# Kernel optimization log

Measured on AMD Instinct MI355X. Metric: run time of the kernel, lower is better.

## Reference

```python
import jax, jax.numpy as jnp
import numpy as np
from jax import lax

EPS = 1e-5


def fps(xyz, npoint):
    # Farthest point sampling; xyz [B, N, 3] -> idx [B, npoint] (starts at point 0)
    B, N, _ = xyz.shape

    def body(carry, _):
        dist, far = carry
        c = jnp.take_along_axis(xyz, far[:, None, None], axis=1)  # [B,1,3]
        d = jnp.sum((xyz - c) ** 2, -1)                            # [B,N]
        dist = jnp.minimum(dist, d)
        nxt = jnp.argmax(dist, -1).astype(jnp.int32)
        return (dist, nxt), far

    init = (jnp.full((B, N), 1e10, xyz.dtype), jnp.zeros((B,), jnp.int32))
    _, idx = lax.scan(body, init, None, length=npoint)
    return idx.T  # [B, npoint]


def query_ball(radius, nsample, xyz, new_xyz):
    # xyz [B,N,3], new_xyz [B,S,3] -> idx [B,S,nsample]
    N = xyz.shape[1]
    sqr = jnp.sum((new_xyz[:, :, None, :] - xyz[:, None, :, :]) ** 2, -1)  # [B,S,N]
    idx = jnp.where(sqr > radius * radius, N, jnp.arange(N)[None, None, :])
    idx = jnp.sort(idx, axis=-1)[:, :, :nsample]
    # out-of-ball slots get replaced by the first in-ball index (torch repo behavior)
    return jnp.where(idx == N, idx[:, :, :1], idx)


def gather_pts(x, idx):
    # x [B,N,C], idx [B,...] -> [B,...,C]
    B = x.shape[0]
    b = jnp.arange(B).reshape((B,) + (1,) * (idx.ndim - 1))
    return x[b, idx]


def mlp_bn(x, layers):
    # x [B,S,K,C]; shared 1x1-conv MLP + training-mode BatchNorm + ReLU
    for w, g, b in layers:
        x = jnp.einsum('bskc,oc->bsko', x, w)
        mean = x.mean((0, 1, 2))
        var = x.var((0, 1, 2))  # biased, as torch BN uses for normalization
        x = jax.nn.relu((x - mean) * lax.rsqrt(var + EPS) * g + b)
    return x


def set_abstraction(xyz, points, npoint, radius, nsample, layers, group_all):
    B = xyz.shape[0]
    if group_all:
        new_xyz = jnp.zeros((B, 1, 3), xyz.dtype)
        new_points = xyz[:, None]  # [B,1,N,3] (raw xyz, no centering)
        if points is not None:
            new_points = jnp.concatenate([new_points, points[:, None]], -1)
    else:
        fidx = fps(xyz, npoint)
        new_xyz = gather_pts(xyz, fidx)                     # [B,S,3]
        idx = query_ball(radius, nsample, xyz, new_xyz)     # [B,S,K]
        grouped = gather_pts(xyz, idx) - new_xyz[:, :, None, :]
        if points is not None:
            new_points = jnp.concatenate([grouped, gather_pts(points, idx)], -1)
        else:
            new_points = grouped
    feat = mlp_bn(new_points, layers).max(2)  # max-pool over neighbors -> [B,S,C]
    return new_xyz, feat


def _forward(xyz_time, l1, l2, l3):
    B, T, N, _ = xyz_time.shape
    x = xyz_time.reshape(B * T, N, 4)
    xyz, t = x[..., :3], x[..., 3:]
    x1_xyz, x1 = set_abstraction(xyz, t, 512, 0.2, 32, l1, False)
    x2_xyz, x2 = set_abstraction(x1_xyz, x1, 128, 0.4, 64, l2, False)
    _, x3 = set_abstraction(x2_xyz, x2, None, None, None, l3, True)
    return x3.reshape(B, T, -1)


def setup_inputs() -> dict:
    key = jax.random.key(0)
    ks = jax.random.split(key, 16)
    inp = {"xyz_time": jax.random.uniform(ks[0], (2, 4, 4096, 4), jnp.float32)}
    specs = {1: [(64, 4), (64, 64), (128, 64)],
             2: [(128, 131), (128, 128), (256, 128)],
             3: [(256, 259), (512, 256), (1024, 512)]}
    i = 1
    for s, layers in specs.items():
        for j, (o, c) in enumerate(layers):
            inp[f"w{s}_{j}"] = jax.random.normal(jax.random.fold_in(ks[i], j), (o, c), jnp.float32) * 0.1
            inp[f"g{s}_{j}"] = jnp.ones((o,), jnp.float32)
            inp[f"b{s}_{j}"] = jnp.zeros((o,), jnp.float32)
        i += 1
    return inp


def reference(xyz_time, w1_0, g1_0, b1_0, w1_1, g1_1, b1_1, w1_2, g1_2, b1_2,
              w2_0, g2_0, b2_0, w2_1, g2_1, b2_1, w2_2, g2_2, b2_2,
              w3_0, g3_0, b3_0, w3_1, g3_1, b3_1, w3_2, g3_2, b3_2):
    l1 = [(w1_0, g1_0, b1_0), (w1_1, g1_1, b1_1), (w1_2, g1_2, b1_2)]
    l2 = [(w2_0, g2_0, b2_0), (w2_1, g2_1, b2_1), (w2_2, g2_2, b2_2)]
    l3 = [(w3_0, g3_0, b3_0), (w3_1, g3_1, b3_1), (w3_2, g3_2, b3_2)]
    return _forward(xyz_time, l1, l2, l3)
```

## Files before the change

### kernel.cpp

```cpp
#include <hip/hip_runtime.h>


typedef short s16x8 __attribute__((ext_vector_type(8)));
typedef float f32x4 __attribute__((ext_vector_type(4)));

__device__ __forceinline__ unsigned short f2bf_rne(float f) {
    unsigned u = __float_as_uint(f);
    u += 0x7FFFu + ((u >> 16) & 1u);
    return (unsigned short)(u >> 16);
}
__device__ __forceinline__ void f2bf_split(float v, unsigned short& hi,
                                           unsigned short& lo) {
    unsigned u = __float_as_uint(v);
    unsigned r = u + 0x7FFFu + ((u >> 16) & 1u);
    hi = (unsigned short)(r >> 16);
    float vh = __uint_as_float(r & 0xFFFF0000u);
    lo = f2bf_rne(v - vh);
}

__device__ __forceinline__ unsigned long long umax64(unsigned long long a,
                                                     unsigned long long b) {
    return a > b ? a : b;
}

__device__ __forceinline__ unsigned wred_umax63(unsigned v) {
    unsigned t;
    t = (unsigned)__builtin_amdgcn_update_dpp(0, (int)v, 0x111, 0xf, 0xf, true); if (t > v) v = t;
    t = (unsigned)__builtin_amdgcn_update_dpp(0, (int)v, 0x112, 0xf, 0xf, true); if (t > v) v = t;
    t = (unsigned)__builtin_amdgcn_update_dpp(0, (int)v, 0x114, 0xf, 0xf, true); if (t > v) v = t;
    t = (unsigned)__builtin_amdgcn_update_dpp(0, (int)v, 0x118, 0xf, 0xf, true); if (t > v) v = t;
    t = (unsigned)__builtin_amdgcn_update_dpp(0, (int)v, 0x142, 0xa, 0xf, true); if (t > v) v = t;
    t = (unsigned)__builtin_amdgcn_update_dpp(0, (int)v, 0x143, 0xc, 0xf, true); if (t > v) v = t;
    return v;
}

__device__ __forceinline__ void wave_argmax(unsigned dbits, unsigned nInv,
                                            unsigned& vmax, unsigned& iInv) {
    unsigned m = wred_umax63(dbits);
    vmax = (unsigned)__builtin_amdgcn_readlane((int)m, 63);
    unsigned cand = (dbits == vmax) ? nInv : 0u;
    unsigned im = wred_umax63(cand);
    iInv = (unsigned)__builtin_amdgcn_readlane((int)im, 63);
}

struct PWArgs {
    const float* w[9];
    unsigned off[9];
    int O[9], C[9], CP[9];
};
__device__ __forceinline__ void prep_w_dev(const PWArgs& a,
                                           unsigned short* __restrict__ wh,
                                           unsigned short* __restrict__ wl,
                                           int i) {
    int l = 0;
#pragma unroll
    for (int k = 1; k < 9; ++k) if (i >= (int)a.off[k]) l = k;
    int li = i - (int)a.off[l];
    int CP = a.CP[l];
    int o = li / CP;
    int c = li - o * CP;
    float v = (c < a.C[l]) ? a.w[l][(size_t)o * a.C[l] + c] : 0.f;
    unsigned short h, lo;
    f2bf_split(v, h, lo);
    wh[i] = h; wl[i] = lo;
}

template<int NT, int ITEMS, int STRIDE>
__global__ __launch_bounds__(NT) void fps_block(
    const float* __restrict__ pts, int npoint,
    int* __restrict__ outIdx, float* __restrict__ outXyz,
    int nFps, PWArgs pw, unsigned short* __restrict__ wh,
    unsigned short* __restrict__ wl, int wtotal)
{
    constexpr int N = NT * ITEMS;
    constexpr int NW = NT / 64;
    __shared__ float4 scoord[N];
    __shared__ unsigned long long wkey[2][NW];

    if (blockIdx.x >= nFps) {
        int i = (blockIdx.x - nFps) * NT + threadIdx.x;
        if (i < wtotal) prep_w_dev(pw, wh, wl, i);
        return;
    }

    const int b = blockIdx.x;
    const int tid = threadIdx.x;
    const int wid = tid >> 6;
    const int lane = tid & 63;
    const float* P = pts + (size_t)b * N * STRIDE;

    float px[ITEMS], py[ITEMS], pz[ITEMS], dloc[ITEMS];
#pragma unroll
    for (int w = 0; w < ITEMS; ++w) {
        int n = tid + w * NT;
        float x, y, z;
        if (STRIDE == 4) {
            float4 v = *(const float4*)(P + (size_t)n * 4);
            x = v.x; y = v.y; z = v.z;
        } else {
            x = P[(size_t)n * STRIDE + 0];
            y = P[(size_t)n * STRIDE + 1];
            z = P[(size_t)n * STRIDE + 2];
        }
        px[w] = x; py[w] = y; pz[w] = z;
        scoord[n] = make_float4(x, y, z, 0.f);
        dloc[w] = 1e10f;
    }
    __syncthreads();
    float4 c0 = scoord[0];
    float cx = c0.x, cy = c0.y, cz = c0.z;
    int far = 0;

    for (int i = 0; i < npoint; ++i) {
        if (tid == 0) {
            outIdx[(size_t)b * npoint + i] = far;
            outXyz[((size_t)b * npoint + i) * 3 + 0] = cx;
            outXyz[((size_t)b * npoint + i) * 3 + 1] = cy;
            outXyz[((size_t)b * npoint + i) * 3 + 2] = cz;
        }
        float bestV = -1.0f;
        int bestW = 0;
#pragma unroll
        for (int w = 0; w < ITEMS; ++w) {
            float dx = __fsub_rn(px[w], cx);
            float dy = __fsub_rn(py[w], cy);
            float dz = __fsub_rn(pz[w], cz);
            float d = __fadd_rn(__fadd_rn(__fmul_rn(dx, dx), __fmul_rn(dy, dy)),
                                __fmul_rn(dz, dz));
            float dd = fminf(dloc[w], d);
            dloc[w] = dd;
            if (dd > bestV) { bestV = dd; bestW = w; }
        }
        int bestN = tid + bestW * NT;
        unsigned vmax, iInv;
        wave_argmax(__float_as_uint(bestV), 0xFFFFFFFFu ^ (unsigned)bestN,
                    vmax, iInv);
        const int par = i & 1;
        if (lane == 0)
            wkey[par][wid] = ((unsigned long long)vmax << 32) | iInv;
        __syncthreads();
        unsigned long long kb = wkey[par][0];
#pragma unroll
        for (int w2 = 1; w2 < NW; ++w2) kb = umax64(kb, wkey[par][w2]);
        far = (int)(0xFFFFFFFFu ^ (unsigned)kb);
        float4 cc = scoord[far];
        cx = cc.x; cy = cc.y; cz = cc.z;
    }
}

__device__ void fps_wave_dev(const float* __restrict__ pts, int npoint,
                             int* __restrict__ outIdx, float* __restrict__ outXyz,
                             int b, float4* scoord)
{
    constexpr int ITEMS = 8;
    constexpr int STRIDE = 3;
    constexpr int N = 64 * ITEMS;
    const int tid = threadIdx.x;
    const float* P = pts + (size_t)b * N * STRIDE;

    float px[ITEMS], py[ITEMS], pz[ITEMS], dloc[ITEMS];
#pragma unroll
    for (int w = 0; w < ITEMS; ++w) {
        int n = tid + w * 64;
        float x = P[(size_t)n * STRIDE + 0];
        float y = P[(size_t)n * STRIDE + 1];
        float z = P[(size_t)n * STRIDE + 2];
        px[w] = x; py[w] = y; pz[w] = z;
        scoord[n] = make_float4(x, y, z, 0.f);
        dloc[w] = 1e10f;
    }
    __threadfence_block();
    float4 c0 = scoord[0];
    float cx = c0.x, cy = c0.y, cz = c0.z;
    int far = 0;

    for (int i = 0; i < npoint; ++i) {
        if (tid == 0) {
            outIdx[(size_t)b * npoint + i] = far;
            outXyz[((size_t)b * npoint + i) * 3 + 0] = cx;
            outXyz[((size_t)b * npoint + i) * 3 + 1] = cy;
            outXyz[((size_t)b * npoint + i) * 3 + 2] = cz;
        }
        float bestV = -1.0f;
        int bestW = 0;
#pragma unroll
        for (int w = 0; w < ITEMS; ++w) {
            float dx = __fsub_rn(px[w], cx);
            float dy = __fsub_rn(py[w], cy);
            float dz = __fsub_rn(pz[w], cz);
            float d = __fadd_rn(__fadd_rn(__fmul_rn(dx, dx), __fmul_rn(dy, dy)),
                                __fmul_rn(dz, dz));
            float dd = fminf(dloc[w], d);
            dloc[w] = dd;
            if (dd > bestV) { bestV = dd; bestW = w; }
        }
        int bestN = tid + bestW * 64;
        unsigned vmax, iInv;
        wave_argmax(__float_as_uint(bestV), 0xFFFFFFFFu ^ (unsigned)bestN,
                    vmax, iInv);
        far = (int)(0xFFFFFFFFu ^ iInv);
        float4 cc = scoord[far];
        cx = cc.x; cy = cc.y; cz = cc.z;
    }
}

__global__ __launch_bounds__(256) void qb_group1(
    const float* __restrict__ xyz ,
    const float* __restrict__ ctr ,
    const float* __restrict__ W0 ,
    float* __restrict__ Yout ,
    double* __restrict__ pS0, double* __restrict__ pQ0,
    int nQb, const float* __restrict__ fpsPts,
    int* __restrict__ fpsIdx, float* __restrict__ fpsXyz)
{
    __shared__ float4 scoord[512];
    __shared__ float4 srows[4][32];
    __shared__ float sstat[4][64][2];
    if ((int)blockIdx.x >= nQb) {
        if (threadIdx.x < 64)
            fps_wave_dev(fpsPts, 128, fpsIdx, fpsXyz,
                         (int)blockIdx.x - nQb, scoord);
        return;
    }
    const int tid = threadIdx.x;
    const int gw = (blockIdx.x * 256 + tid) >> 6;
    const int wid = tid >> 6;
    const int lane = tid & 63;
    int b = gw >> 9;
    const float* P = xyz + (size_t)b * 4096 * 4;
    float cx = ctr[(size_t)gw * 3 + 0];
    float cy = ctr[(size_t)gw * 3 + 1];
    float cz = ctr[(size_t)gw * 3 + 2];
    int cnt = 0;
    float f0x = 0.f, f0y = 0.f, f0z = 0.f, f0t = 0.f;
    bool haveFirst = false;
    for (int base = 0; base < 4096 && cnt < 32; base += 64) {
        int n = base + lane;
        float4 p = *(const float4*)(P + (size_t)n * 4);
        float ex = __fsub_rn(p.x, cx);
        float ey = __fsub_rn(p.y, cy);
        float ez = __fsub_rn(p.z, cz);
        float d = __fadd_rn(__fadd_rn(__fmul_rn(ex, ex), __fmul_rn(ey, ey)),
                            __fmul_rn(ez, ez));
        bool inb = !(d > 0.04f);
        unsigned long long mask = __ballot(inb);
        if (mask) {
            if (!haveFirst) {
                int fl = (int)__builtin_ctzll(mask);
                f0x = __shfl(ex, fl); f0y = __shfl(ey, fl);
                f0z = __shfl(ez, fl); f0t = __shfl(p.w, fl);
                haveFirst = true;
            }
            if (inb) {
                int pos = cnt + __builtin_popcountll(mask & ((1ull << lane) - 1ull));
                if (pos < 32)
                    srows[wid][pos] = make_float4(ex, ey, ez, p.w);
            }
            cnt += (int)__builtin_popcountll(mask);
        }
    }
    if (cnt > 32) cnt = 32;
    for (int p2 = cnt + lane; p2 < 32; p2 += 64)
        srows[wid][p2] = make_float4(f0x, f0y, f0z, f0t);
    __syncthreads();

    float wc0 = W0[lane * 4 + 0];
    float wc1 = W0[lane * 4 + 1];
    float wc2 = W0[lane * 4 + 2];
    float wc3 = W0[lane * 4 + 3];
    float s = 0.f, s2 = 0.f;
    float* yp = Yout + (size_t)gw * 32 * 64 + lane;
#pragma unroll 4
    for (int r = 0; r < 32; ++r) {
        float4 e = srows[wid][r];
        float y = e.x * wc0 + e.y * wc1 + e.z * wc2 + e.w * wc3;
        yp[(size_t)r * 64] = y;
        s += y;
        s2 += y * y;
    }
    sstat[wid][lane][0] = s;
    sstat[wid][lane][1] = s2;
    __syncthreads();
    if (tid < 64) {
        double S = 0.0, S2 = 0.0;
#pragma unroll
        for (int w2 = 0; w2 < 4; ++w2) {
            S += (double)sstat[w2][tid][0];
            S2 += (double)sstat[w2][tid][1];
        }
        atomicAdd(&pS0[tid], S);
        atomicAdd(&pQ0[tid], S2);
    }
}

__device__ __forceinline__ void qb2_dev(
    const float* __restrict__ xyz, const float* __restrict__ centers,
    int* __restrict__ outIdx, int gw, int lane)
{
    const int N = 512, stride = 3, S = 128, nsample = 64;
    const float r2 = 0.16f;
    int b = gw / S;
    const float* P = xyz + (size_t)b * N * stride;
    float cx = centers[(size_t)gw * 3 + 0];
    float cy = centers[(size_t)gw * 3 + 1];
    float cz = centers[(size_t)gw * 3 + 2];
    int* out = outIdx + (size_t)gw * nsample;
    int cnt = 0;
    int firstIdx = 0;
    bool haveFirst = false;
    for (int base = 0; base < N && cnt < nsample; base += 64) {
        int n = base + lane;
        bool inb = false;
        if (n < N) {
            float dx = __fsub_rn(cx, P[(size_t)n * stride + 0]);
            float dy = __fsub_rn(cy, P[(size_t)n * stride + 1]);
            float dz = __fsub_rn(cz, P[(size_t)n * stride + 2]);
            float d = __fadd_rn(__fadd_rn(__fmul_rn(dx, dx), __fmul_rn(dy, dy)),
                                __fmul_rn(dz, dz));
            inb = !(d > r2);
        }
        unsigned long long mask = __ballot(inb);
        if (mask) {
            if (!haveFirst) { firstIdx = base + __builtin_ctzll(mask); haveFirst = true; }
            if (inb) {
                int pos = cnt + __builtin_popcountll(mask & ((1ull << lane) - 1ull));
                if (pos < nsample) out[pos] = n;
            }
            cnt += (int)__builtin_popcountll(mask);
        }
    }
    if (cnt > nsample) cnt = nsample;
    for (int p = cnt + lane; p < nsample; p += 64) out[p] = firstIdx;
}

__global__ __launch_bounds__(256) void gemm_fused(
    const float* __restrict__ X,
    const double* __restrict__ pSin, const double* __restrict__ pQin,
    const float* __restrict__ gIn, const float* __restrict__ bIn,
    double invMin, int actMode, int bnCh,
    const unsigned short* __restrict__ Bh, const unsigned short* __restrict__ Bl,
    float* __restrict__ Y,
    double* __restrict__ pSout, double* __restrict__ pQout,
    int AC, int CPW, int O, int gmode,
    const int* __restrict__ gqb, const float* __restrict__ gxyz,
    const float* __restrict__ gctr, const float* __restrict__ gfeat,
    const float* __restrict__ gfmin,
    int redK, float* __restrict__ Vmax, float* __restrict__ Vmin,
    int nMain, const float* __restrict__ qbXyz,
    const float* __restrict__ qbCtr, int* __restrict__ qbOut)
{
    constexpr int PITCH = 40;
    __shared__ __align__(16) unsigned short sAh[128 * PITCH];
    __shared__ __align__(16) unsigned short sAl[128 * PITCH];
    __shared__ __align__(16) unsigned short sBh[128 * PITCH];
    __shared__ __align__(16) unsigned short sBl[128 * PITCH];
    __shared__ float sred[2048];
    __shared__ float sScale[512];
    __shared__ float sShift[512];

    if ((int)blockIdx.x >= nMain) {
        int wid = threadIdx.x >> 6, lane = threadIdx.x & 63;
        int gw = ((int)blockIdx.x - nMain) * 4 + wid;
        if (gw < 1024) qb2_dev(qbXyz, qbCtr, qbOut, gw, lane);
        return;
    }

    const int tid = threadIdx.x;
    const int lane = tid & 63;
    const int wid = tid >> 6;
    const int col15 = lane & 15;
    const int quad = lane >> 4;
    const int wm = (wid >> 1) * 64;
    const int wo = (wid & 1) * 64;
    const int m0 = blockIdx.x * 128;
    const int o0 = blockIdx.y * 128;
    const int lr = tid >> 2;
    const int lc = (tid & 3) * 8;

    if (bnCh > 0) {
        for (int c = tid; c < bnCh; c += 256) {
            double S = pSin[c], Q = pQin[c];
            double mean = S * invMin;
            double var = Q * invMin - mean * mean;
            float varf = (float)var;
            if (varf < 0.f) varf = 0.f;
            float sc = gIn[c] * rsqrtf(varf + 1e-5f);
            sScale[c] = sc;
            sShift[c] = bIn[c] - (float)mean * sc;
        }
    }
    __syncthreads();

    f32x4 acc[4][4];
#pragma unroll
    for (int mt = 0; mt < 4; ++mt)
#pragma unroll
        for (int ot = 0; ot < 4; ++ot)
            acc[mt][ot] = {0.f, 0.f, 0.f, 0.f};

    for (int k0 = 0; k0 < CPW; k0 += 32) {
#pragma unroll
        for (int it = 0; it < 2; ++it) {
            int r = lr + it * 64;
            int c = k0 + lc;
            unsigned short h[8], l[8];
            float vv[8];
            bool have = true;
            if (gmode == 0) {
                if (c + 8 <= AC) {
                    const float* xr = X + (size_t)(m0 + r) * AC + c;
                    float4 v0 = *(const float4*)xr;
                    float4 v1 = *(const float4*)(xr + 4);
                    vv[0] = v0.x; vv[1] = v0.y; vv[2] = v0.z; vv[3] = v0.w;
                    vv[4] = v1.x; vv[5] = v1.y; vv[6] = v1.z; vv[7] = v1.w;
                    if (actMode == 1) {
#pragma unroll
                        for (int j = 0; j < 8; ++j)
                            vv[j] = fmaxf(vv[j] * sScale[c + j] + sShift[c + j], 0.f);
                    }
                } else {
                    have = false;
                }
            } else if (gmode == 2) {
                int m = m0 + r;
                int idx = gqb[m];
                idx = (idx < 0) ? 0 : (idx > 511 ? 511 : idx);
                int bb2 = m >> 13;
                int bs = m >> 6;
                int ctrg = bb2 * 512 + idx;
                const float* fmx = gfeat + (size_t)ctrg * 128;
                const float* fmn = gfmin + (size_t)ctrg * 128;
                const float* xrow = gxyz + (size_t)ctrg * 3;
                const float* crow = gctr + (size_t)bs * 3;
#pragma unroll
                for (int j = 0; j < 8; ++j) {
                    int cc = c + j;
                    float v = 0.f;
                    if (cc < 3)        v = __fsub_rn(xrow[cc], crow[cc]);
                    else if (cc < 131) {
                        int fc = cc - 3;
                        float sc = sScale[fc];
                        float sel = (sc >= 0.f) ? fmx[fc] : fmn[fc];
                        v = fmaxf(sel * sc + sShift[fc], 0.f);
                    }
                    vv[j] = v;
                }
            } else {
                int m = m0 + r;
                const float* fmx = gfeat + (size_t)m * 256;
                const float* fmn = gfmin + (size_t)m * 256;
                const float* crow = gctr + (size_t)m * 3;
#pragma unroll
                for (int j = 0; j < 8; ++j) {
                    int cc = c + j;
                    float v = 0.f;
                    if (cc < 3)        v = crow[cc];
                    else if (cc < 259) {
                        int fc = cc - 3;
                        float sc = sScale[fc];
                        float sel = (sc >= 0.f) ? fmx[fc] : fmn[fc];
                        v = fmaxf(sel * sc + sShift[fc], 0.f);
                    }
                    vv[j] = v;
                }
            }
            if (have) {
#pragma unroll
                for (int j = 0; j < 8; ++j) f2bf_split(vv[j], h[j], l[j]);
            } else {
#pragma unroll
                for (int j = 0; j < 8; ++j) { h[j] = 0; l[j] = 0; }
            }
            *(ushort4*)&sAh[r * PITCH + lc] = make_ushort4(h[0], h[1], h[2], h[3]);
            *(ushort4*)&sAh[r * PITCH + lc + 4] = make_ushort4(h[4], h[5], h[6], h[7]);
            *(ushort4*)&sAl[r * PITCH + lc] = make_ushort4(l[0], l[1], l[2], l[3]);
            *(ushort4*)&sAl[r * PITCH + lc + 4] = make_ushort4(l[4], l[5], l[6], l[7]);
        }
#pragma unroll
        for (int it = 0; it < 2; ++it) {
            int r = lr + it * 64;
            int c = k0 + lc;
            int o = o0 + r;
            uint4 vh = {0, 0, 0, 0}, vl = {0, 0, 0, 0};
            if (o < O && c < CPW) {
                size_t goff = (size_t)o * CPW + c;
                vh = *(const uint4*)(Bh + goff);
                vl = *(const uint4*)(Bl + goff);
            }
            *(uint4*)&sBh[r * PITCH + lc] = vh;
            *(uint4*)&sBl[r * PITCH + lc] = vl;
        }
        __syncthreads();
        s16x8 ah[4], al[4], bh[4], bl[4];
#pragma unroll
        for (int mt = 0; mt < 4; ++mt) {
            int rowoff = (wm + mt * 16 + col15) * PITCH + quad * 8;
            ah[mt] = *(const s16x8*)&sAh[rowoff];
            al[mt] = *(const s16x8*)&sAl[rowoff];
        }
#pragma unroll
        for (int ot = 0; ot < 4; ++ot) {
            int rowoff = (wo + ot * 16 + col15) * PITCH + quad * 8;
            bh[ot] = *(const s16x8*)&sBh[rowoff];
            bl[ot] = *(const s16x8*)&sBl[rowoff];
        }
#pragma unroll
        for (int mt = 0; mt < 4; ++mt)
#pragma unroll
            for (int ot = 0; ot < 4; ++ot) {
                acc[mt][ot] = __builtin_amdgcn_mfma_f32_16x16x32_bf16(
                    ah[mt], bl[ot], acc[mt][ot], 0, 0, 0);
                acc[mt][ot] = __builtin_amdgcn_mfma_f32_16x16x32_bf16(
                    al[mt], bh[ot], acc[mt][ot], 0, 0, 0);
                acc[mt][ot] = __builtin_amdgcn_mfma_f32_16x16x32_bf16(
                    ah[mt], bh[ot], acc[mt][ot], 0, 0, 0);
            }
        __syncthreads();
    }
    if (redK == 0) {
#pragma unroll
        for (int mt = 0; mt < 4; ++mt)
#pragma unroll
            for (int ot = 0; ot < 4; ++ot) {
                int og = o0 + wo + ot * 16 + col15;
                if (og < O) {
#pragma unroll
                    for (int r = 0; r < 4; ++r) {
                        int mg = m0 + wm + mt * 16 + quad * 4 + r;
                        Y[(size_t)mg * O + og] = acc[mt][ot][r];
                    }
                }
            }
    } else if (redK == 32) {
#pragma unroll
        for (int ot = 0; ot < 4; ++ot) {
            int og = o0 + wo + ot * 16 + col15;
#pragma unroll
            for (int cp = 0; cp < 2; ++cp) {
                float mx = acc[2 * cp][ot][0];
                float mn = mx;
#pragma unroll
                for (int mi = 0; mi < 2; ++mi)
#pragma unroll
                    for (int r = 0; r < 4; ++r) {
                        float v = acc[2 * cp + mi][ot][r];
                        mx = fmaxf(mx, v);
                        mn = fminf(mn, v);
                    }
                mx = fmaxf(mx, __shfl_xor(mx, 16));
                mx = fmaxf(mx, __shfl_xor(mx, 32));
                mn = fminf(mn, __shfl_xor(mn, 16));
                mn = fminf(mn, __shfl_xor(mn, 32));
                if (quad == 0) {
                    int ctr = (m0 >> 5) + (wm >> 5) + cp;
                    Vmax[(size_t)ctr * O + og] = mx;
                    Vmin[(size_t)ctr * O + og] = mn;
                }
            }
        }
    } else {
#pragma unroll
        for (int ot = 0; ot < 4; ++ot) {
            int og = o0 + wo + ot * 16 + col15;
            float mx = acc[0][ot][0];
            float mn = mx;
#pragma unroll
            for (int mt = 0; mt < 4; ++mt)
#pragma unroll
                for (int r = 0; r < 4; ++r) {
                    float v = acc[mt][ot][r];
                    mx = fmaxf(mx, v);
                    mn = fminf(mn, v);
                }
            mx = fmaxf(mx, __shfl_xor(mx, 16));
            mx = fmaxf(mx, __shfl_xor(mx, 32));
            mn = fminf(mn, __shfl_xor(mn, 16));
            mn = fminf(mn, __shfl_xor(mn, 32));
            if (quad == 0) {
                int ctr = (m0 >> 6) + (wm >> 6);
                Vmax[(size_t)ctr * O + og] = mx;
                Vmin[(size_t)ctr * O + og] = mn;
            }
        }
    }
#pragma unroll
    for (int ot = 0; ot < 4; ++ot) {
        float s = 0.f, s2 = 0.f;
#pragma unroll
        for (int mt = 0; mt < 4; ++mt)
#pragma unroll
            for (int r = 0; r < 4; ++r) {
                float v = acc[mt][ot][r];
                s += v;
                s2 += v * v;
            }
        int slot = ((wid * 4 + quad) * 16 + col15) * 4 + ot;
        sred[slot * 2] = s;
        sred[slot * 2 + 1] = s2;
    }
    __syncthreads();
    if (tid < 128) {
        int col = tid;
        int o = o0 + col;
        if (o < O) {
            int cb = col >> 6;
            int ot = (col & 63) >> 4;
            int c15 = col & 15;
            double S = 0.0, S2 = 0.0;
#pragma unroll
            for (int wp = 0; wp < 2; ++wp) {
                int wd = cb + wp * 2;
#pragma unroll
                for (int q = 0; q < 4; ++q) {
                    int slot = ((wd * 4 + q) * 16 + c15) * 4 + ot;
                    S += (double)sred[slot * 2];
                    S2 += (double)sred[slot * 2 + 1];
                }
            }
            atomicAdd(&pSout[o], S);
            atomicAdd(&pQout[o], S2);
        }
    }
}

__global__ __launch_bounds__(256) void bn_relu_max(
    const float* __restrict__ Y,
    const double* __restrict__ pS, const double* __restrict__ pQ,
    const float* __restrict__ gv, const float* __restrict__ bv, double invM,
    float* __restrict__ out, int Stot, int K, int O)
{
    int idx = blockIdx.x * 256 + threadIdx.x;
    if (idx >= Stot * O) return;
    int s = idx / O;
    int o = idx - s * O;
    double S = pS[o], Q = pQ[o];
    double mean = S * invM;
    double var = Q * invM - mean * mean;
    float varf = (float)var;
    if (varf < 0.f) varf = 0.f;
    float sc = gv[o] * rsqrtf(varf + 1e-5f);
    float sh = bv[o] - (float)mean * sc;
    const float* basep = Y + (size_t)s * K * O + o;
    float mx = 0.f;
    for (int k = 0; k < K; ++k) {
        float v = basep[(size_t)k * O] * sc + sh;
        v = fmaxf(v, 0.f);
        mx = fmaxf(mx, v);
    }
    out[idx] = mx;
}

extern "C" void kernel_launch(void* const* d_in, const int* in_sizes, int n_in,
                              void* d_out, int out_size, void* d_ws, size_t ws_size,
                              hipStream_t stream)
{
    const float* xin = (const float*)d_in[0];
    const float* w[9]; const float* g[9]; const float* bb[9];
    for (int i = 0; i < 9; ++i) {
        w[i]  = (const float*)d_in[1 + 3 * i];
        g[i]  = (const float*)d_in[2 + 3 * i];
        bb[i] = (const float*)d_in[3 + 3 * i];
    }

    char* base = (char*)d_ws;
    size_t off = 0;
    auto alloc = [&](size_t bytes) -> void* {
        void* p = base + off;
        off = (off + bytes + 255) & ~(size_t)255;
        return p;
    };
    const int OC[9][3] = {{64,4,8},{64,64,64},{128,64,64},
                          {128,131,136},{128,128,128},{256,128,128},
                          {256,259,264},{512,256,256},{1024,512,512}};
    size_t woff[10]; woff[0] = 0;
    for (int i = 0; i < 9; ++i) woff[i + 1] = woff[i] + (size_t)OC[i][0] * OC[i][2];

    int*    fps1   = (int*)alloc((size_t)4096 * 4);
    int*    fps2   = (int*)alloc((size_t)1024 * 4);
    int*    qb2    = (int*)alloc((size_t)65536 * 4);
    float*  nx1    = (float*)alloc((size_t)12288 * 4);
    float*  nx2    = (float*)alloc((size_t)3072 * 4);
    double* partS  = (double*)alloc((size_t)9 * 1024 * 8);
    double* partQ  = (double*)alloc((size_t)9 * 1024 * 8);
    unsigned short* WH = (unsigned short*)alloc(woff[9] * 2);
    unsigned short* WL = (unsigned short*)alloc(woff[9] * 2);
    const size_t zeroBytes = off;
    float*  XG = (float*)alloc((size_t)65536 * 136 * 4);
    float*  A  = (float*)alloc((size_t)16777216 * 4);
    if (off > ws_size) return;

    hipMemsetAsync(d_ws, 0, zeroBytes, stream);

    PWArgs pwa;
    for (int i = 0; i < 9; ++i) {
        pwa.w[i] = w[i]; pwa.off[i] = (unsigned)woff[i];
        pwa.O[i] = OC[i][0]; pwa.C[i] = OC[i][1]; pwa.CP[i] = OC[i][2];
    }
    const int nPrep = (int)((woff[9] + 255) / 256);

    auto gemm = [&](const float* X, int prevLi, double invMprev, int actMode,
                    int bnCh, int li, float* Y, int YB, int OB, int AC,
                    int CPW, int O, int gmode, const int* gqb,
                    const float* gxyz, const float* gctr, const float* gfeat,
                    const float* gfmin, int redK, float* Vmax, float* Vmin,
                    int extraQB, const float* qx, const float* qc, int* qo) {
        gemm_fused<<<dim3(YB + extraQB, OB), 256, 0, stream>>>(
            X,
            prevLi >= 0 ? partS + (size_t)prevLi * 1024 : nullptr,
            prevLi >= 0 ? partQ + (size_t)prevLi * 1024 : nullptr,
            prevLi >= 0 ? g[prevLi] : nullptr,
            prevLi >= 0 ? bb[prevLi] : nullptr,
            invMprev, actMode, bnCh,
            WH + woff[li], WL + woff[li], Y,
            partS + (size_t)li * 1024, partQ + (size_t)li * 1024,
            AC, CPW, O, gmode, gqb, gxyz, gctr, gfeat, gfmin,
            redK, Vmax, Vmin, YB, qx, qc, qo);
    };

    const double inv1 = 1.0 / 131072.0;
    const double inv2 = 1.0 / 65536.0;
    const double inv3 = 1.0 / 1024.0;

    fps_block<256, 16, 4><<<8 + nPrep, 256, 0, stream>>>(
        xin, 512, fps1, nx1, 8, pwa, WH, WL, (int)woff[9]);
    qb_group1<<<1024 + 8, 256, 0, stream>>>(
        xin, nx1, w[0], A, partS + 0, partQ + 0, 1024, nx1, fps2, nx2);

    gemm(A, 0, inv1, 1, 64, 1, XG, 1024, 1, 64, 64, 64, 0,
         nullptr, nullptr, nullptr, nullptr, nullptr, 0, nullptr, nullptr,
         256, nx1, nx2, qb2);
    gemm(XG, 1, inv1, 1, 64, 2, A, 1024, 1, 64, 64, 128, 0,
         nullptr, nullptr, nullptr, nullptr, nullptr, 32, A, A + 524288,
         0, nullptr, nullptr, nullptr);

    gemm(nullptr, 2, inv1, 2, 128, 3, XG, 512, 1, 136, 136, 128, 2,
         qb2, nx1, nx2, A, A + 524288, 0, nullptr, nullptr,
         0, nullptr, nullptr, nullptr);
    gemm(XG, 3, inv2, 1, 128, 4, A, 512, 1, 128, 128, 128, 0,
         nullptr, nullptr, nullptr, nullptr, nullptr, 0, nullptr, nullptr,
         0, nullptr, nullptr, nullptr);
    gemm(A, 4, inv2, 1, 128, 5, XG, 512, 2, 128, 128, 256, 0,
         nullptr, nullptr, nullptr, nullptr, nullptr, 64, XG, XG + 262144,
         0, nullptr, nullptr, nullptr);

    gemm(nullptr, 5, inv2, 2, 256, 6, A, 8, 2, 264, 264, 256, 3,
         nullptr, nullptr, nx2, XG, XG + 262144, 0, nullptr, nullptr,
         0, nullptr, nullptr, nullptr);
    gemm(A, 6, inv3, 1, 256, 7, XG, 8, 4, 256, 256, 512, 0,
         nullptr, nullptr, nullptr, nullptr, nullptr, 0, nullptr, nullptr,
         0, nullptr, nullptr, nullptr);
    gemm(XG, 7, inv3, 1, 512, 8, A, 8, 8, 512, 512, 1024, 0,
         nullptr, nullptr, nullptr, nullptr, nullptr, 0, nullptr, nullptr,
         0, nullptr, nullptr, nullptr);
    bn_relu_max<<<(8 * 1024) / 256, 256, 0, stream>>>(
        A, partS + 8 * 1024, partQ + 8 * 1024, g[8], bb[8], inv3,
        (float*)d_out, 8, 128, 1024);
}
```

Baseline: 774.7 us.

## Fuse SA3 GEMM chain and final max into one cooperative kernel

Replaces the three SA3 MLP GEMM launches and the BN-ReLU-max launch with a single cooperative kernel of 64 blocks. Grid-wide syncs separate the stages, and each block loops over output tiles. This removes per-launch overhead and idle gaps between the small SA3 kernels. The cost is fewer blocks per stage, grid.sync overhead, and a fallback to the old launches if the cooperative launch fails.

```diff
diff --git a/kernel.cpp b/kernel.cpp
--- a/kernel.cpp
+++ b/kernel.cpp
@@ -1,4 +1,7 @@
 #include <hip/hip_runtime.h>
+#include <hip/hip_cooperative_groups.h>
+
+namespace cg = cooperative_groups;
 
 
 typedef short s16x8 __attribute__((ext_vector_type(8)));
@@ -623,6 +626,259 @@
     }
 }
 
+__device__ void sa3_gemm(
+    const float* __restrict__ X,
+    const double* __restrict__ pSin, const double* __restrict__ pQin,
+    const float* __restrict__ gIn, const float* __restrict__ bIn,
+    double invMin, int bnCh, int gmode,
+    const float* __restrict__ gctr, const float* __restrict__ gfeat,
+    const float* __restrict__ gfmin,
+    const unsigned short* __restrict__ Bh, const unsigned short* __restrict__ Bl,
+    float* __restrict__ Y, double* __restrict__ pSout, double* __restrict__ pQout,
+    int AC, int CPW, int O, int YB, int ntile, int G,
+    unsigned short* sAh, unsigned short* sAl,
+    unsigned short* sBh, unsigned short* sBl,
+    float* sred, float* sScale, float* sShift)
+{
+    constexpr int PITCH = 40;
+    const int tid = threadIdx.x;
+    const int lane = tid & 63;
+    const int wid = tid >> 6;
+    const int col15 = lane & 15;
+    const int quad = lane >> 4;
+    const int wm = (wid >> 1) * 64;
+    const int wo = (wid & 1) * 64;
+    const int lr = tid >> 2;
+    const int lc = (tid & 3) * 8;
+
+    for (int c = tid; c < bnCh; c += 256) {
+        double S = pSin[c], Q = pQin[c];
+        double mean = S * invMin;
+        double var = Q * invMin - mean * mean;
+        float varf = (float)var;
+        if (varf < 0.f) varf = 0.f;
+        float sc = gIn[c] * rsqrtf(varf + 1e-5f);
+        sScale[c] = sc;
+        sShift[c] = bIn[c] - (float)mean * sc;
+    }
+    __syncthreads();
+
+    for (int t = blockIdx.x; t < ntile; t += G) {
+        const int m0 = (t % YB) * 128;
+        const int o0 = (t / YB) * 128;
+        f32x4 acc[4][4];
+#pragma unroll
+        for (int mt = 0; mt < 4; ++mt)
+#pragma unroll
+            for (int ot = 0; ot < 4; ++ot) acc[mt][ot] = {0.f, 0.f, 0.f, 0.f};
+
+        for (int k0 = 0; k0 < CPW; k0 += 32) {
+#pragma unroll
+            for (int it = 0; it < 2; ++it) {
+                int r = lr + it * 64;
+                int c = k0 + lc;
+                unsigned short h[8], l[8];
+                float vv[8];
+                bool have = true;
+                if (gmode == 0) {
+                    if (c + 8 <= AC) {
+                        const float* xr = X + (size_t)(m0 + r) * AC + c;
+                        float4 v0 = *(const float4*)xr;
+                        float4 v1 = *(const float4*)(xr + 4);
+                        vv[0] = v0.x; vv[1] = v0.y; vv[2] = v0.z; vv[3] = v0.w;
+                        vv[4] = v1.x; vv[5] = v1.y; vv[6] = v1.z; vv[7] = v1.w;
+#pragma unroll
+                        for (int j = 0; j < 8; ++j)
+                            vv[j] = fmaxf(vv[j] * sScale[c + j] + sShift[c + j], 0.f);
+                    } else {
+                        have = false;
+                    }
+                } else {
+                    int m = m0 + r;
+                    const float* fmx = gfeat + (size_t)m * 256;
+                    const float* fmn = gfmin + (size_t)m * 256;
+                    const float* crow = gctr + (size_t)m * 3;
+#pragma unroll
+                    for (int j = 0; j < 8; ++j) {
+                        int cc = c + j;
+                        float v = 0.f;
+                        if (cc < 3)        v = crow[cc];
+                        else if (cc < 259) {
+                            int fc = cc - 3;
+                            float sc = sScale[fc];
+                            float sel = (sc >= 0.f) ? fmx[fc] : fmn[fc];
+                            v = fmaxf(sel * sc + sShift[fc], 0.f);
+                        }
+                        vv[j] = v;
+                    }
+                }
+                if (have) {
+#pragma unroll
+                    for (int j = 0; j < 8; ++j) f2bf_split(vv[j], h[j], l[j]);
+                } else {
+#pragma unroll
+                    for (int j = 0; j < 8; ++j) { h[j] = 0; l[j] = 0; }
+                }
+                *(ushort4*)&sAh[r * PITCH + lc] = make_ushort4(h[0], h[1], h[2], h[3]);
+                *(ushort4*)&sAh[r * PITCH + lc + 4] = make_ushort4(h[4], h[5], h[6], h[7]);
+                *(ushort4*)&sAl[r * PITCH + lc] = make_ushort4(l[0], l[1], l[2], l[3]);
+                *(ushort4*)&sAl[r * PITCH + lc + 4] = make_ushort4(l[4], l[5], l[6], l[7]);
+            }
+#pragma unroll
+            for (int it = 0; it < 2; ++it) {
+                int r = lr + it * 64;
+                int c = k0 + lc;
+                int o = o0 + r;
+                uint4 vh = {0, 0, 0, 0}, vl = {0, 0, 0, 0};
+                if (o < O && c < CPW) {
+                    size_t goff = (size_t)o * CPW + c;
+                    vh = *(const uint4*)(Bh + goff);
+                    vl = *(const uint4*)(Bl + goff);
+                }
+                *(uint4*)&sBh[r * PITCH + lc] = vh;
+                *(uint4*)&sBl[r * PITCH + lc] = vl;
+            }
+            __syncthreads();
+            s16x8 ah[4], al[4], bh[4], bl[4];
+#pragma unroll
+            for (int mt = 0; mt < 4; ++mt) {
+                int rowoff = (wm + mt * 16 + col15) * PITCH + quad * 8;
+                ah[mt] = *(const s16x8*)&sAh[rowoff];
+                al[mt] = *(const s16x8*)&sAl[rowoff];
+            }
+#pragma unroll
+            for (int ot = 0; ot < 4; ++ot) {
+                int rowoff = (wo + ot * 16 + col15) * PITCH + quad * 8;
+                bh[ot] = *(const s16x8*)&sBh[rowoff];
+                bl[ot] = *(const s16x8*)&sBl[rowoff];
+            }
+#pragma unroll
+            for (int mt = 0; mt < 4; ++mt)
+#pragma unroll
+                for (int ot = 0; ot < 4; ++ot) {
+                    acc[mt][ot] = __builtin_amdgcn_mfma_f32_16x16x32_bf16(
+                        ah[mt], bl[ot], acc[mt][ot], 0, 0, 0);
+                    acc[mt][ot] = __builtin_amdgcn_mfma_f32_16x16x32_bf16(
+                        al[mt], bh[ot], acc[mt][ot], 0, 0, 0);
+                    acc[mt][ot] = __builtin_amdgcn_mfma_f32_16x16x32_bf16(
+                        ah[mt], bh[ot], acc[mt][ot], 0, 0, 0);
+                }
+            __syncthreads();
+        }
+#pragma unroll
+        for (int mt = 0; mt < 4; ++mt)
+#pragma unroll
+            for (int ot = 0; ot < 4; ++ot) {
+                int og = o0 + wo + ot * 16 + col15;
+                if (og < O) {
+#pragma unroll
+                    for (int r = 0; r < 4; ++r) {
+                        int mg = m0 + wm + mt * 16 + quad * 4 + r;
+                        Y[(size_t)mg * O + og] = acc[mt][ot][r];
+                    }
+                }
+            }
+#pragma unroll
+        for (int ot = 0; ot < 4; ++ot) {
+            float s = 0.f, s2 = 0.f;
+#pragma unroll
+            for (int mt = 0; mt < 4; ++mt)
+#pragma unroll
+                for (int r = 0; r < 4; ++r) {
+                    float v = acc[mt][ot][r];
+                    s += v;
+                    s2 += v * v;
+                }
+            int slot = ((wid * 4 + quad) * 16 + col15) * 4 + ot;
+            sred[slot * 2] = s;
+            sred[slot * 2 + 1] = s2;
+        }
+        __syncthreads();
+        if (tid < 128) {
+            int col = tid;
+            int o = o0 + col;
+            if (o < O) {
+                int cb = col >> 6;
+                int ot = (col & 63) >> 4;
+                int c15 = col & 15;
+                double S = 0.0, S2 = 0.0;
+#pragma unroll
+                for (int wp = 0; wp < 2; ++wp) {
+                    int wd = cb + wp * 2;
+#pragma unroll
+                    for (int q = 0; q < 4; ++q) {
+                        int slot = ((wd * 4 + q) * 16 + c15) * 4 + ot;
+                        S += (double)sred[slot * 2];
+                        S2 += (double)sred[slot * 2 + 1];
+                    }
+                }
+                atomicAdd(&pSout[o], S);
+                atomicAdd(&pQout[o], S2);
+            }
+        }
+        __syncthreads();
+    }
+}
+
+struct SA3Args {
+    const float* nx2; const float* Vmax2; const float* Vmin2;
+    const unsigned short *Bh6, *Bl6, *Bh7, *Bl7, *Bh8, *Bl8;
+    double *pS5, *pQ5, *pS6, *pQ6, *pS7, *pQ7, *pS8, *pQ8;
+    const float *g5, *b5, *g6, *b6, *g7, *b7, *g8, *b8;
+    float *bufA, *bufB, *bufC, *out;
+    double inv2, inv3;
+};
+
+__global__ __launch_bounds__(256) void sa3_coop(SA3Args a)
+{
+    constexpr int PITCH = 40;
+    __shared__ __align__(16) unsigned short sAh[128 * PITCH];
+    __shared__ __align__(16) unsigned short sAl[128 * PITCH];
+    __shared__ __align__(16) unsigned short sBh[128 * PITCH];
+    __shared__ __align__(16) unsigned short sBl[128 * PITCH];
+    __shared__ float sred[2048];
+    __shared__ float sScale[512];
+    __shared__ float sShift[512];
+    cg::grid_group grid = cg::this_grid();
+    const int G = gridDim.x;
+
+    sa3_gemm(nullptr, a.pS5, a.pQ5, a.g5, a.b5, a.inv2, 256, 3,
+             a.nx2, a.Vmax2, a.Vmin2, a.Bh6, a.Bl6,
+             a.bufA, a.pS6, a.pQ6, 264, 264, 256, 8, 16, G,
+             sAh, sAl, sBh, sBl, sred, sScale, sShift);
+    grid.sync();
+    sa3_gemm(a.bufA, a.pS6, a.pQ6, a.g6, a.b6, a.inv3, 256, 0,
+             nullptr, nullptr, nullptr, a.Bh7, a.Bl7,
+             a.bufB, a.pS7, a.pQ7, 256, 256, 512, 8, 32, G,
+             sAh, sAl, sBh, sBl, sred, sScale, sShift);
+    grid.sync();
+    sa3_gemm(a.bufB, a.pS7, a.pQ7, a.g7, a.b7, a.inv3, 512, 0,
+             nullptr, nullptr, nullptr, a.Bh8, a.Bl8,
+             a.bufC, a.pS8, a.pQ8, 512, 512, 1024, 8, 64, G,
+             sAh, sAl, sBh, sBl, sred, sScale, sShift);
+    grid.sync();
+    for (int idx = blockIdx.x * 256 + threadIdx.x; idx < 8 * 1024;
+         idx += G * 256) {
+        int s = idx >> 10;
+        int o = idx & 1023;
+        double S = a.pS8[o], Q = a.pQ8[o];
+        double mean = S * a.inv3;
+        double var = Q * a.inv3 - mean * mean;
+        float varf = (float)var;
+        if (varf < 0.f) varf = 0.f;
+        float sc = a.g8[o] * rsqrtf(varf + 1e-5f);
+        float sh = a.b8[o] - (float)mean * sc;
+        const float* basep = a.bufC + (size_t)s * 128 * 1024 + o;
+        float mx = 0.f;
+        for (int k = 0; k < 128; ++k) {
+            float v = basep[(size_t)k * 1024] * sc + sh;
+            v = fmaxf(v, 0.f);
+            mx = fmaxf(mx, v);
+        }
+        a.out[idx] = mx;
+    }
+}
+
 __global__ __launch_bounds__(256) void bn_relu_max(
     const float* __restrict__ Y,
     const double* __restrict__ pS, const double* __restrict__ pQ,
@@ -743,16 +999,37 @@
          nullptr, nullptr, nullptr, nullptr, nullptr, 64, XG, XG + 262144,
          0, nullptr, nullptr, nullptr);
 
-    gemm(nullptr, 5, inv2, 2, 256, 6, A, 8, 2, 264, 264, 256, 3,
-         nullptr, nullptr, nx2, XG, XG + 262144, 0, nullptr, nullptr,
-         0, nullptr, nullptr, nullptr);
-    gemm(A, 6, inv3, 1, 256, 7, XG, 8, 4, 256, 256, 512, 0,
-         nullptr, nullptr, nullptr, nullptr, nullptr, 0, nullptr, nullptr,
-         0, nullptr, nullptr, nullptr);
-    gemm(XG, 7, inv3, 1, 512, 8, A, 8, 8, 512, 512, 1024, 0,
-         nullptr, nullptr, nullptr, nullptr, nullptr, 0, nullptr, nullptr,
-         0, nullptr, nullptr, nullptr);
-    bn_relu_max<<<(8 * 1024) / 256, 256, 0, stream>>>(
-        A, partS + 8 * 1024, partQ + 8 * 1024, g[8], bb[8], inv3,
-        (float*)d_out, 8, 128, 1024);
-}
+    {
+        SA3Args s{};
+        s.nx2 = nx2; s.Vmax2 = XG; s.Vmin2 = XG + 262144;
+        s.Bh6 = WH + woff[6]; s.Bl6 = WL + woff[6];
+        s.Bh7 = WH + woff[7]; s.Bl7 = WL + woff[7];
+        s.Bh8 = WH + woff[8]; s.Bl8 = WL + woff[8];
+        s.pS5 = partS + 5 * 1024; s.pQ5 = partQ + 5 * 1024;
+        s.pS6 = partS + 6 * 1024; s.pQ6 = partQ + 6 * 1024;
+        s.pS7 = partS + 7 * 1024; s.pQ7 = partQ + 7 * 1024;
+        s.pS8 = partS + 8 * 1024; s.pQ8 = partQ + 8 * 1024;
+        s.g5 = g[5]; s.b5 = bb[5]; s.g6 = g[6]; s.b6 = bb[6];
+        s.g7 = g[7]; s.b7 = bb[7]; s.g8 = g[8]; s.b8 = bb[8];
+        s.bufA = A; s.bufB = A + 262144; s.bufC = A + 786432;
+        s.out = (float*)d_out;
+        s.inv2 = inv2; s.inv3 = inv3;
+        void* ka[] = {(void*)&s};
+        hipError_t ce = hipLaunchCooperativeKernel(
+            (const void*)sa3_coop, dim3(64), dim3(256), ka, 0, stream);
+        if (ce != hipSuccess) {
+            gemm(nullptr, 5, inv2, 2, 256, 6, A, 8, 2, 264, 264, 256, 3,
+                 nullptr, nullptr, nx2, XG, XG + 262144, 0, nullptr, nullptr,
+                 0, nullptr, nullptr, nullptr);
+            gemm(A, 6, inv3, 1, 256, 7, XG, 8, 4, 256, 256, 512, 0,
+                 nullptr, nullptr, nullptr, nullptr, nullptr, 0, nullptr, nullptr,
+                 0, nullptr, nullptr, nullptr);
+            gemm(XG, 7, inv3, 1, 512, 8, A, 8, 8, 512, 512, 1024, 0,
+                 nullptr, nullptr, nullptr, nullptr, nullptr, 0, nullptr, nullptr,
+                 0, nullptr, nullptr, nullptr);
+            bn_relu_max<<<(8 * 1024) / 256, 256, 0, stream>>>(
+                A, partS + 8 * 1024, partQ + 8 * 1024, g[8], bb[8], inv3,
+                (float*)d_out, 8, 128, 1024);
+        }
+    }
+}
```

Measured after the change: 823.3 us. 1.06x slower.
